# Kernel optimization log

Measured on AMD Instinct MI355X. Metric: run time of the kernel, lower is better.

The kernel has to match this reference:

```python
import jax, jax.numpy as jnp
import numpy as np

B, S, H, C = 128, 2048, 1024, 256
N_LANGS = 8


def setup_inputs() -> dict:
    key = jax.random.key(0)
    ks = jax.random.split(key, 7)
    features = jax.random.normal(ks[0], (B, S, H), dtype=jnp.float32)
    language_ids = jax.random.randint(ks[1], (B,), 0, N_LANGS, dtype=jnp.int64)
    attention_mask = jnp.ones((B, S), dtype=jnp.int32)
    # projection MLP params (stored as [in, out]; math-equivalent to torch Linear)
    W1 = jax.random.normal(ks[2], (H, H), dtype=jnp.float32) / np.sqrt(H)
    b1 = jnp.zeros((H,), dtype=jnp.float32)
    W2 = jax.random.normal(ks[3], (H, C), dtype=jnp.float32) / np.sqrt(H)
    b2 = jnp.zeros((C,), dtype=jnp.float32)
    temperature = jnp.array([0.07], dtype=jnp.float32)
    return {"features": features, "W1": W1, "b1": b1, "W2": W2, "b2": b2,
            "temperature": temperature, "language_ids": language_ids,
            "attention_mask": attention_mask}


def reference(features, W1, b1, W2, b2, temperature, language_ids, attention_mask):
    # masked mean pool over seq: [B,S,H] -> [B,H]
    m = attention_mask.astype(features.dtype)[:, :, None]
    pooled = (features * m).sum(axis=1) / m.sum(axis=1)
    # MLP projection head
    h = jax.nn.relu(pooled @ W1 + b1)
    proj = h @ W2 + b2
    # L2 normalize (torch F.normalize eps=1e-12)
    norm = jnp.maximum(jnp.linalg.norm(proj, axis=-1, keepdims=True), 1e-12)
    proj = proj / norm
    # similarity matrix [B,B]
    sim = (proj @ proj.T) / temperature[0]
    # vectorized replacement of the O(B^2) python label loop
    b = language_ids.shape[0]
    diff_lang = language_ids[:, None] != language_ids[None, :]
    off_diag = ~jnp.eye(b, dtype=bool)
    labels = (diff_lang & off_diag).astype(sim.dtype)
    # torch F.cross_entropy with soft (probability) targets:
    # mean over rows of -sum_j labels[i,j] * log_softmax(sim)[i,j]
    logp = jax.nn.log_softmax(sim, axis=-1)
    loss = jnp.mean(-(labels * logp).sum(axis=-1))
    return proj, loss
```

## Files before the change

kernel.cpp:

```cpp
#include <hip/hip_runtime.h>
#include <math.h>

#define BATCH 128
#define SEQ   2048
#define HID   1024
#define CDIM  256
#define SPLIT 16
#define ROWS_PER (SEQ / SPLIT)
#define KC1   16
#define KC2   4

typedef float vf4 __attribute__((ext_vector_type(4)));
typedef int   vi4 __attribute__((ext_vector_type(4)));

__global__ __launch_bounds__(256) void pool_partial_kernel(
    const float* __restrict__ feat, const int* __restrict__ mask,
    float* __restrict__ partial)
{
    const int b     = blockIdx.x;
    const int chunk = blockIdx.y;
    const int t     = threadIdx.x;

    const vf4* fp = reinterpret_cast<const vf4*>(feat) +
                    ((size_t)b * SEQ + (size_t)chunk * ROWS_PER) * (HID / 4);
    const vi4* mp = reinterpret_cast<const vi4*>(
                        mask + (size_t)b * SEQ + (size_t)chunk * ROWS_PER);

    vf4 acc = {0.f, 0.f, 0.f, 0.f};
    for (int s = 0; s < ROWS_PER; s += 8) {
        const vi4 m0 = mp[s / 4];
        const vi4 m1 = mp[s / 4 + 1];
        float mm[8];
        mm[0] = (float)m0.x; mm[1] = (float)m0.y; mm[2] = (float)m0.z; mm[3] = (float)m0.w;
        mm[4] = (float)m1.x; mm[5] = (float)m1.y; mm[6] = (float)m1.z; mm[7] = (float)m1.w;
        #pragma unroll
        for (int u = 0; u < 8; ++u) {
            const vf4 v = __builtin_nontemporal_load(&fp[(size_t)(s + u) * (HID / 4) + t]);
            acc += v * mm[u];
        }
    }
    reinterpret_cast<vf4*>(partial)[((size_t)b * SPLIT + chunk) * (HID / 4) + t] = acc;
}

__global__ __launch_bounds__(256) void pool_final_kernel(
    const float* __restrict__ partial, const int* __restrict__ mask,
    float* __restrict__ pooled)
{
    const int b  = blockIdx.x;
    const int cc = blockIdx.y;
    const int t  = threadIdx.x;

    int local = 0;
    #pragma unroll
    for (int s = t; s < SEQ; s += 256) local += mask[(size_t)b * SEQ + s];
    __shared__ int redi[256];
    redi[t] = local;
    __syncthreads();
    for (int off = 128; off > 0; off >>= 1) {
        if (t < off) redi[t] += redi[t + off];
        __syncthreads();
    }
    const float inv = 1.0f / (float)redi[0];

    const int col = cc * 256 + t;
    float a = 0.f;
    #pragma unroll
    for (int c = 0; c < SPLIT; ++c)
        a += partial[((size_t)b * SPLIT + c) * HID + col];
    pooled[(size_t)b * HID + col] = a * inv;
}

__global__ __launch_bounds__(256) void mlp1_partial_kernel(
    const float* __restrict__ pooled, const float* __restrict__ W1,
    float* __restrict__ part1)
{
    const int jc = blockIdx.x;
    const int bg = blockIdx.y;
    const int kc = blockIdx.z;
    const int t  = threadIdx.x;

    __shared__ float ps[8][64];
    if (t < 128) {
        const int r = t >> 4;
        const int c = (t & 15) * 4;
        *reinterpret_cast<vf4*>(&ps[r][c]) =
            *reinterpret_cast<const vf4*>(&pooled[(size_t)(bg * 8 + r) * HID + kc * 64 + c]);
    }
    __syncthreads();

    const int j = jc * 256 + t;
    const float* w = W1 + (size_t)(kc * 64) * HID + j;

    float acc[8];
    #pragma unroll
    for (int r = 0; r < 8; ++r) acc[r] = 0.f;

    #pragma unroll
    for (int k = 0; k < 64; k += 8) {
        float wv[8];
        #pragma unroll
        for (int u = 0; u < 8; ++u) wv[u] = w[(size_t)(k + u) * HID];
        #pragma unroll
        for (int u = 0; u < 8; ++u) {
            #pragma unroll
            for (int r = 0; r < 8; ++r)
                acc[r] = fmaf(ps[r][k + u], wv[u], acc[r]);
        }
    }
    #pragma unroll
    for (int r = 0; r < 8; ++r)
        part1[((size_t)kc * BATCH + bg * 8 + r) * HID + j] = acc[r];
}

__global__ __launch_bounds__(256) void mlp2_partial_kernel(
    const float* __restrict__ part1, const float* __restrict__ b1,
    const float* __restrict__ W2, float* __restrict__ part2)
{
    const int b  = blockIdx.x;
    const int kc = blockIdx.y;
    const int t  = threadIdx.x;

    __shared__ float hs[256];
    float s = b1[kc * 256 + t];
    #pragma unroll
    for (int p = 0; p < KC1; ++p)
        s += part1[((size_t)p * BATCH + b) * HID + kc * 256 + t];
    hs[t] = fmaxf(s, 0.f);
    __syncthreads();

    const float* w = W2 + (size_t)(kc * 256) * CDIM + t;
    float acc = 0.f;
    #pragma unroll
    for (int k = 0; k < 256; k += 8) {
        float wv[8];
        #pragma unroll
        for (int u = 0; u < 8; ++u) wv[u] = w[(size_t)(k + u) * CDIM];
        #pragma unroll
        for (int u = 0; u < 8; ++u) acc = fmaf(hs[k + u], wv[u], acc);
    }
    part2[((size_t)kc * BATCH + b) * CDIM + t] = acc;
}

__global__ __launch_bounds__(256) void mlp2_final_kernel(
    const float* __restrict__ part2, const float* __restrict__ b2,
    float* __restrict__ proj)
{
    const int b = blockIdx.x;
    const int t = threadIdx.x;

    float acc = b2[t];
    #pragma unroll
    for (int p = 0; p < KC2; ++p)
        acc += part2[((size_t)p * BATCH + b) * CDIM + t];

    __shared__ float red[CDIM];
    red[t] = acc * acc;
    __syncthreads();
    for (int off = CDIM / 2; off > 0; off >>= 1) {
        if (t < off) red[t] += red[t + off];
        __syncthreads();
    }
    const float norm = fmaxf(sqrtf(red[0]), 1e-12f);
    proj[(size_t)b * CDIM + t] = acc / norm;
}

__global__ __launch_bounds__(128) void sim_loss_kernel(
    const float* __restrict__ proj, const float* __restrict__ temp,
    const int* __restrict__ lang, float* __restrict__ loss_part)
{
    const int i = blockIdx.x;
    const int j = threadIdx.x;

    __shared__ float pi[CDIM];
    if (j < CDIM / 4)
        reinterpret_cast<vf4*>(pi)[j] =
            reinterpret_cast<const vf4*>(proj + (size_t)i * CDIM)[j];
    __syncthreads();

    const vf4* pj = reinterpret_cast<const vf4*>(proj + (size_t)j * CDIM);
    float acc = 0.f;
    #pragma unroll 8
    for (int c = 0; c < CDIM / 4; ++c) {
        const vf4 v = pj[c];
        acc = fmaf(pi[4 * c + 0], v.x, acc);
        acc = fmaf(pi[4 * c + 1], v.y, acc);
        acc = fmaf(pi[4 * c + 2], v.z, acc);
        acc = fmaf(pi[4 * c + 3], v.w, acc);
    }
    const float s = acc / temp[0];
    const int li = lang[i];

    __shared__ float r1[BATCH];
    __shared__ int   ci[BATCH];

    r1[j] = s;
    __syncthreads();
    for (int off = BATCH / 2; off > 0; off >>= 1) {
        if (j < off) r1[j] = fmaxf(r1[j], r1[j + off]);
        __syncthreads();
    }
    const float m = r1[0];
    __syncthreads();

    r1[j] = expf(s - m);
    __syncthreads();
    for (int off = BATCH / 2; off > 0; off >>= 1) {
        if (j < off) r1[j] += r1[j + off];
        __syncthreads();
    }
    const float lse = m + logf(r1[0]);
    __syncthreads();

    const bool sel = (lang[j] != li) && (j != i);
    r1[j] = sel ? s : 0.f;
    ci[j] = sel ? 1 : 0;
    __syncthreads();
    for (int off = BATCH / 2; off > 0; off >>= 1) {
        if (j < off) { r1[j] += r1[j + off]; ci[j] += ci[j + off]; }
        __syncthreads();
    }
    if (j == 0) loss_part[i] = (float)ci[0] * lse - r1[0];
}

__global__ __launch_bounds__(128) void loss_reduce_kernel(
    const float* __restrict__ loss_part, float* __restrict__ out)
{
    const int t = threadIdx.x;
    __shared__ float red[BATCH];
    red[t] = loss_part[t];
    __syncthreads();
    for (int off = BATCH / 2; off > 0; off >>= 1) {
        if (t < off) red[t] += red[t + off];
        __syncthreads();
    }
    if (t == 0) out[0] = red[0] / (float)BATCH;
}

extern "C" void kernel_launch(void* const* d_in, const int* in_sizes, int n_in,
                              void* d_out, int out_size, void* d_ws, size_t ws_size,
                              hipStream_t stream)
{
    const float* feat = (const float*)d_in[0];
    const float* W1   = (const float*)d_in[1];
    const float* b1   = (const float*)d_in[2];
    const float* W2   = (const float*)d_in[3];
    const float* b2   = (const float*)d_in[4];
    const float* temp = (const float*)d_in[5];
    const int*   lang = (const int*)d_in[6];
    const int*   amask= (const int*)d_in[7];
    float* out = (float*)d_out;
    float* ws  = (float*)d_ws;

    float* partial   = ws;
    float* pooled    = partial + (size_t)BATCH * SPLIT * HID;
    float* part1     = pooled + (size_t)BATCH * HID;
    float* part2     = part1 + (size_t)KC1 * BATCH * HID;
    float* loss_part = part2 + (size_t)KC2 * BATCH * CDIM;

    pool_partial_kernel<<<dim3(BATCH, SPLIT), 256, 0, stream>>>(feat, amask, partial);
    pool_final_kernel<<<dim3(BATCH, 4), 256, 0, stream>>>(partial, amask, pooled);
    mlp1_partial_kernel<<<dim3(HID / 256, BATCH / 8, KC1), 256, 0, stream>>>(pooled, W1, part1);
    mlp2_partial_kernel<<<dim3(BATCH, KC2), 256, 0, stream>>>(part1, b1, W2, part2);
    mlp2_final_kernel<<<BATCH, CDIM, 0, stream>>>(part2, b2, out);
    sim_loss_kernel<<<BATCH, BATCH, 0, stream>>>(out, temp, lang, loss_part);
    loss_reduce_kernel<<<1, BATCH, 0, stream>>>(loss_part, out + (size_t)BATCH * CDIM);
}
```

Before: 206.8 us.

## Fuse pooling finalize, MLP2 split-K and loss reduction to cut kernel launches

Drops the pool_final, mlp2_final and loss_reduce kernels. The mask count is now computed per chunk in the pooling pass, and the sum over partial chunks is folded into the MLP1 input staging. MLP2 runs as a single 1024-thread block per row that reduces its four K-slices in shared memory and normalizes in place. The final loss mean uses a last-block atomic counter in the similarity kernel. This removes launches and intermediate global round trips, at the cost of MLP1 blocks re-reading the 16 partial rows redundantly and of relying on a counter reset written inside the first kernel.

```diff
diff --git a/kernel.cpp b/kernel.cpp
--- a/kernel.cpp
+++ b/kernel.cpp
@@ -8,14 +8,14 @@
 #define SPLIT 16
 #define ROWS_PER (SEQ / SPLIT)
 #define KC1   16
-#define KC2   4
 
 typedef float vf4 __attribute__((ext_vector_type(4)));
 typedef int   vi4 __attribute__((ext_vector_type(4)));
 
 __global__ __launch_bounds__(256) void pool_partial_kernel(
     const float* __restrict__ feat, const int* __restrict__ mask,
-    float* __restrict__ partial)
+    float* __restrict__ partial, int* __restrict__ cntp,
+    unsigned* __restrict__ counter)
 {
     const int b     = blockIdx.x;
     const int chunk = blockIdx.y;
@@ -27,9 +27,11 @@
                         mask + (size_t)b * SEQ + (size_t)chunk * ROWS_PER);
 
     vf4 acc = {0.f, 0.f, 0.f, 0.f};
+    int csum = 0;
     for (int s = 0; s < ROWS_PER; s += 8) {
         const vi4 m0 = mp[s / 4];
         const vi4 m1 = mp[s / 4 + 1];
+        csum += m0.x + m0.y + m0.z + m0.w + m1.x + m1.y + m1.z + m1.w;
         float mm[8];
         mm[0] = (float)m0.x; mm[1] = (float)m0.y; mm[2] = (float)m0.z; mm[3] = (float)m0.w;
         mm[4] = (float)m1.x; mm[5] = (float)m1.y; mm[6] = (float)m1.z; mm[7] = (float)m1.w;
@@ -40,39 +42,15 @@
         }
     }
     reinterpret_cast<vf4*>(partial)[((size_t)b * SPLIT + chunk) * (HID / 4) + t] = acc;
-}
-
-__global__ __launch_bounds__(256) void pool_final_kernel(
-    const float* __restrict__ partial, const int* __restrict__ mask,
-    float* __restrict__ pooled)
-{
-    const int b  = blockIdx.x;
-    const int cc = blockIdx.y;
-    const int t  = threadIdx.x;
-
-    int local = 0;
-    #pragma unroll
-    for (int s = t; s < SEQ; s += 256) local += mask[(size_t)b * SEQ + s];
-    __shared__ int redi[256];
-    redi[t] = local;
-    __syncthreads();
-    for (int off = 128; off > 0; off >>= 1) {
-        if (t < off) redi[t] += redi[t + off];
-        __syncthreads();
-    }
-    const float inv = 1.0f / (float)redi[0];
-
-    const int col = cc * 256 + t;
-    float a = 0.f;
-    #pragma unroll
-    for (int c = 0; c < SPLIT; ++c)
-        a += partial[((size_t)b * SPLIT + c) * HID + col];
-    pooled[(size_t)b * HID + col] = a * inv;
-}
-
-__global__ __launch_bounds__(256) void mlp1_partial_kernel(
-    const float* __restrict__ pooled, const float* __restrict__ W1,
-    float* __restrict__ part1)
+    if (t == 0) {
+        cntp[b * SPLIT + chunk] = csum;
+        if (b == 0 && chunk == 0) *counter = 0u;
+    }
+}
+
+__global__ __launch_bounds__(256) void mlp1_fused_kernel(
+    const float* __restrict__ partial, const int* __restrict__ cntp,
+    const float* __restrict__ W1, float* __restrict__ part1)
 {
     const int jc = blockIdx.x;
     const int bg = blockIdx.y;
@@ -80,12 +58,28 @@
     const int t  = threadIdx.x;
 
     __shared__ float ps[8][64];
+    __shared__ float invs[8];
+
+    if (t < 8) {
+        const int* cp = cntp + (size_t)(bg * 8 + t) * SPLIT;
+        int c = 0;
+        #pragma unroll
+        for (int p = 0; p < SPLIT; ++p) c += cp[p];
+        invs[t] = 1.0f / (float)c;
+    }
+
+    const int r  = t >> 4;
+    const int c4 = t & 15;
+    vf4 acc4 = {0.f, 0.f, 0.f, 0.f};
     if (t < 128) {
-        const int r = t >> 4;
-        const int c = (t & 15) * 4;
-        *reinterpret_cast<vf4*>(&ps[r][c]) =
-            *reinterpret_cast<const vf4*>(&pooled[(size_t)(bg * 8 + r) * HID + kc * 64 + c]);
-    }
+        const vf4* pp = reinterpret_cast<const vf4*>(partial);
+        #pragma unroll
+        for (int p = 0; p < SPLIT; ++p)
+            acc4 += pp[((size_t)(bg * 8 + r) * SPLIT + p) * (HID / 4) + kc * 16 + c4];
+    }
+    __syncthreads();
+    if (t < 128)
+        *reinterpret_cast<vf4*>(&ps[r][c4 * 4]) = acc4 * invs[r];
     __syncthreads();
 
     const int j = jc * 256 + t;
@@ -93,7 +87,7 @@
 
     float acc[8];
     #pragma unroll
-    for (int r = 0; r < 8; ++r) acc[r] = 0.f;
+    for (int rr = 0; rr < 8; ++rr) acc[rr] = 0.f;
 
     #pragma unroll
     for (int k = 0; k < 64; k += 8) {
@@ -103,32 +97,38 @@
         #pragma unroll
         for (int u = 0; u < 8; ++u) {
             #pragma unroll
-            for (int r = 0; r < 8; ++r)
-                acc[r] = fmaf(ps[r][k + u], wv[u], acc[r]);
+            for (int rr = 0; rr < 8; ++rr)
+                acc[rr] = fmaf(ps[rr][k + u], wv[u], acc[rr]);
         }
     }
     #pragma unroll
-    for (int r = 0; r < 8; ++r)
-        part1[((size_t)kc * BATCH + bg * 8 + r) * HID + j] = acc[r];
-}
-
-__global__ __launch_bounds__(256) void mlp2_partial_kernel(
+    for (int rr = 0; rr < 8; ++rr)
+        part1[((size_t)kc * BATCH + bg * 8 + rr) * HID + j] = acc[rr];
+}
+
+__global__ __launch_bounds__(1024) void mlp2_full_kernel(
     const float* __restrict__ part1, const float* __restrict__ b1,
-    const float* __restrict__ W2, float* __restrict__ part2)
+    const float* __restrict__ W2, const float* __restrict__ b2,
+    float* __restrict__ proj)
 {
     const int b  = blockIdx.x;
-    const int kc = blockIdx.y;
     const int t  = threadIdx.x;
-
-    __shared__ float hs[256];
-    float s = b1[kc * 256 + t];
+    const int j  = t & 255;
+    const int kc = t >> 8;
+
+    __shared__ float hs[HID];
+    __shared__ float pacc[4][CDIM];
+    __shared__ float red[CDIM];
+
+    float s = b1[t];
     #pragma unroll
     for (int p = 0; p < KC1; ++p)
-        s += part1[((size_t)p * BATCH + b) * HID + kc * 256 + t];
+        s += part1[((size_t)p * BATCH + b) * HID + t];
     hs[t] = fmaxf(s, 0.f);
     __syncthreads();
 
-    const float* w = W2 + (size_t)(kc * 256) * CDIM + t;
+    const float* w = W2 + (size_t)(kc * 256) * CDIM + j;
+    const float* h = hs + kc * 256;
     float acc = 0.f;
     #pragma unroll
     for (int k = 0; k < 256; k += 8) {
@@ -136,37 +136,31 @@
         #pragma unroll
         for (int u = 0; u < 8; ++u) wv[u] = w[(size_t)(k + u) * CDIM];
         #pragma unroll
-        for (int u = 0; u < 8; ++u) acc = fmaf(hs[k + u], wv[u], acc);
-    }
-    part2[((size_t)kc * BATCH + b) * CDIM + t] = acc;
-}
-
-__global__ __launch_bounds__(256) void mlp2_final_kernel(
-    const float* __restrict__ part2, const float* __restrict__ b2,
-    float* __restrict__ proj)
-{
-    const int b = blockIdx.x;
-    const int t = threadIdx.x;
-
-    float acc = b2[t];
-    #pragma unroll
-    for (int p = 0; p < KC2; ++p)
-        acc += part2[((size_t)p * BATCH + b) * CDIM + t];
-
-    __shared__ float red[CDIM];
-    red[t] = acc * acc;
+        for (int u = 0; u < 8; ++u) acc = fmaf(h[k + u], wv[u], acc);
+    }
+    pacc[kc][j] = acc;
+    __syncthreads();
+
+    float tot = 0.f;
+    if (t < CDIM) {
+        tot = b2[t] + pacc[0][t] + pacc[1][t] + pacc[2][t] + pacc[3][t];
+        red[t] = tot * tot;
+    }
     __syncthreads();
     for (int off = CDIM / 2; off > 0; off >>= 1) {
         if (t < off) red[t] += red[t + off];
         __syncthreads();
     }
-    const float norm = fmaxf(sqrtf(red[0]), 1e-12f);
-    proj[(size_t)b * CDIM + t] = acc / norm;
+    if (t < CDIM) {
+        const float norm = fmaxf(sqrtf(red[0]), 1e-12f);
+        proj[(size_t)b * CDIM + t] = tot / norm;
+    }
 }
 
 __global__ __launch_bounds__(128) void sim_loss_kernel(
     const float* __restrict__ proj, const float* __restrict__ temp,
-    const int* __restrict__ lang, float* __restrict__ loss_part)
+    const int* __restrict__ lang, float* __restrict__ loss_part,
+    unsigned* __restrict__ counter, float* __restrict__ out_loss)
 {
     const int i = blockIdx.x;
     const int j = threadIdx.x;
@@ -219,21 +213,25 @@
         if (j < off) { r1[j] += r1[j + off]; ci[j] += ci[j + off]; }
         __syncthreads();
     }
-    if (j == 0) loss_part[i] = (float)ci[0] * lse - r1[0];
-}
-
-__global__ __launch_bounds__(128) void loss_reduce_kernel(
-    const float* __restrict__ loss_part, float* __restrict__ out)
-{
-    const int t = threadIdx.x;
-    __shared__ float red[BATCH];
-    red[t] = loss_part[t];
-    __syncthreads();
-    for (int off = BATCH / 2; off > 0; off >>= 1) {
-        if (t < off) red[t] += red[t + off];
-        __syncthreads();
-    }
-    if (t == 0) out[0] = red[0] / (float)BATCH;
+
+    __shared__ bool last;
+    if (j == 0) {
+        loss_part[i] = (float)ci[0] * lse - r1[0];
+        __threadfence();
+        const unsigned old = atomicAdd(counter, 1u);
+        last = (old == BATCH - 1);
+    }
+    __syncthreads();
+    if (last) {
+        __threadfence();
+        r1[j] = loss_part[j];
+        __syncthreads();
+        for (int off = BATCH / 2; off > 0; off >>= 1) {
+            if (j < off) r1[j] += r1[j + off];
+            __syncthreads();
+        }
+        if (j == 0) out_loss[0] = r1[0] / (float)BATCH;
+    }
 }
 
 extern "C" void kernel_launch(void* const* d_in, const int* in_sizes, int n_in,
@@ -251,17 +249,17 @@
     float* out = (float*)d_out;
     float* ws  = (float*)d_ws;
 
-    float* partial   = ws;
-    float* pooled    = partial + (size_t)BATCH * SPLIT * HID;
-    float* part1     = pooled + (size_t)BATCH * HID;
-    float* part2     = part1 + (size_t)KC1 * BATCH * HID;
-    float* loss_part = part2 + (size_t)KC2 * BATCH * CDIM;
-
-    pool_partial_kernel<<<dim3(BATCH, SPLIT), 256, 0, stream>>>(feat, amask, partial);
-    pool_final_kernel<<<dim3(BATCH, 4), 256, 0, stream>>>(partial, amask, pooled);
-    mlp1_partial_kernel<<<dim3(HID / 256, BATCH / 8, KC1), 256, 0, stream>>>(pooled, W1, part1);
-    mlp2_partial_kernel<<<dim3(BATCH, KC2), 256, 0, stream>>>(part1, b1, W2, part2);
-    mlp2_final_kernel<<<BATCH, CDIM, 0, stream>>>(part2, b2, out);
-    sim_loss_kernel<<<BATCH, BATCH, 0, stream>>>(out, temp, lang, loss_part);
-    loss_reduce_kernel<<<1, BATCH, 0, stream>>>(loss_part, out + (size_t)BATCH * CDIM);
-}
+    float*    partial   = ws;
+    float*    part1     = partial + (size_t)BATCH * SPLIT * HID;
+    float*    loss_part = part1 + (size_t)KC1 * BATCH * HID;
+    int*      cntp      = (int*)(loss_part + BATCH);
+    unsigned* counter   = (unsigned*)(cntp + BATCH * SPLIT);
+
+    pool_partial_kernel<<<dim3(BATCH, SPLIT), 256, 0, stream>>>(
+        feat, amask, partial, cntp, counter);
+    mlp1_fused_kernel<<<dim3(HID / 256, BATCH / 8, KC1), 256, 0, stream>>>(
+        partial, cntp, W1, part1);
+    mlp2_full_kernel<<<BATCH, 1024, 0, stream>>>(part1, b1, W2, b2, out);
+    sim_loss_kernel<<<BATCH, BATCH, 0, stream>>>(
+        out, temp, lang, loss_part, counter, out + (size_t)BATCH * CDIM);
+}
```

Result: no change. 210.5 us (+1.8%).
